# Optimization experiments

Hardware: AMD Instinct MI355X
Metric: run time of the kernel (lower is better)

The kernel has to match this reference:

```python
import jax, jax.numpy as jnp
import numpy as np

H = 64
IN_DIM = 32
N = 50000
E = 100000
B = 500


def setup_inputs() -> dict:
    key = jax.random.key(0)
    ks = jax.random.split(key, 16)
    def rn(k, shape, s=0.05):
        return jax.random.normal(k, shape, dtype=jnp.float32) * s
    inp = dict(
        nfeat=rn(ks[0], (N, IN_DIM), 1.0),
        efeat=rn(ks[1], (E, 5), 1.0),
        lin0_w=rn(ks[2], (IN_DIM, H)), lin0_b=jnp.zeros((H,), jnp.float32),
        ew1=rn(ks[3], (5, 128)), eb1=jnp.zeros((128,), jnp.float32),
        ew2=rn(ks[4], (128, H * H)), eb2=jnp.zeros((H * H,), jnp.float32),
        conv_b=jnp.zeros((H,), jnp.float32),
        gru_wih=rn(ks[5], (3 * H, H)), gru_whh=rn(ks[6], (3 * H, H)),
        gru_bih=jnp.zeros((3 * H,), jnp.float32), gru_bhh=jnp.zeros((3 * H,), jnp.float32),
        lstm_wih=rn(ks[7], (4 * H, 2 * H)), lstm_whh=rn(ks[8], (4 * H, H)),
        lstm_bih=jnp.zeros((4 * H,), jnp.float32), lstm_bhh=jnp.zeros((4 * H,), jnp.float32),
        fc1_w=rn(ks[9], (2 * H, H)), fc1_b=jnp.zeros((H,), jnp.float32),
        fc2_w=rn(ks[10], (H, 1)), fc2_b=jnp.zeros((1,), jnp.float32),
        src=jax.random.randint(ks[11], (E,), 0, N),
        dst=jax.random.randint(ks[12], (E,), 0, N),
        graph_id=jnp.arange(N) // (N // B),  # B graphs of equal size, sorted
        num_graphs=B,
    )
    return inp


def reference(nfeat, efeat, lin0_w, lin0_b, ew1, eb1, ew2, eb2, conv_b,
              gru_wih, gru_whh, gru_bih, gru_bhh,
              lstm_wih, lstm_whh, lstm_bih, lstm_bhh,
              fc1_w, fc1_b, fc2_w, fc2_b,
              src, dst, graph_id, num_graphs):
    n_nodes = nfeat.shape[0]
    # lin0 + relu
    h = jax.nn.relu(nfeat @ lin0_w + lin0_b)  # [N, H]
    # edge-conditioned weight matrices (same for all 3 iterations)
    We = (jax.nn.relu(efeat @ ew1 + eb1) @ ew2 + eb2).reshape(-1, H, H)  # [E, H, H]
    deg = jnp.maximum(
        jax.ops.segment_sum(jnp.ones(src.shape[0], jnp.float32), dst, num_segments=n_nodes), 1.0)
    for _ in range(3):
        # NNConv: gather src feats, per-edge matmul, scatter-mean at dst
        msg = jnp.einsum('eh,eho->eo', h[src], We)  # [E, H]
        agg = jax.ops.segment_sum(msg, dst, num_segments=n_nodes) / deg[:, None]
        m = jax.nn.relu(agg + conv_b)
        # GRU step (PyTorch gate order r,z,n)
        gi = m @ gru_wih.T + gru_bih
        gh = h @ gru_whh.T + gru_bhh
        r = jax.nn.sigmoid(gi[:, :H] + gh[:, :H])
        z = jax.nn.sigmoid(gi[:, H:2 * H] + gh[:, H:2 * H])
        n = jnp.tanh(gi[:, 2 * H:] + r * gh[:, 2 * H:])
        h = (1.0 - z) * n + z * h
    feat = h  # [N, H]
    # Set2Set pooling: 3 iters, 1-layer LSTM with input 2H
    q_star = jnp.zeros((num_graphs, 2 * H), jnp.float32)
    hh = jnp.zeros((num_graphs, H), jnp.float32)
    cc = jnp.zeros((num_graphs, H), jnp.float32)
    for _ in range(3):
        gates = q_star @ lstm_wih.T + lstm_bih + hh @ lstm_whh.T + lstm_bhh
        i = jax.nn.sigmoid(gates[:, :H])
        f = jax.nn.sigmoid(gates[:, H:2 * H])
        g = jnp.tanh(gates[:, 2 * H:3 * H])
        o = jax.nn.sigmoid(gates[:, 3 * H:])
        cc = f * cc + i * g
        hh = o * jnp.tanh(cc)
        q = hh  # [B, H]
        e = jnp.sum(feat * q[graph_id], axis=-1)  # [N]
        emax = jax.ops.segment_max(e, graph_id, num_segments=num_graphs)
        alpha = jnp.exp(e - emax[graph_id])
        denom = jax.ops.segment_sum(alpha, graph_id, num_segments=num_graphs)
        alpha = alpha / denom[graph_id]
        readout = jax.ops.segment_sum(alpha[:, None] * feat, graph_id, num_segments=num_graphs)
        q_star = jnp.concatenate([q, readout], axis=-1)  # [B, 2H]
    pred = jax.nn.relu(q_star @ fc1_w + fc1_b) @ fc2_w + fc2_b  # [B, 1]
    return pred.reshape(-1)
```

## Files before the change

kernel.cpp:

```cpp
#include <hip/hip_runtime.h>

#define HD 64
#define NNODE 50000
#define NEDGE 100000
#define NGR 500
#define NPG 100
#define EPAD 100352
#define NCH 66
#define NUPL 65

typedef _Float16 f16;
typedef _Float16 f16x2 __attribute__((ext_vector_type(2)));
typedef _Float16 f16x8 __attribute__((ext_vector_type(8)));
typedef float f32x4 __attribute__((ext_vector_type(4)));

__device__ __forceinline__ float sigmoidf_(float x) { return 1.f / (1.f + __expf(-x)); }

__device__ __forceinline__ void gload16(const void* g, void* l) {
    __builtin_amdgcn_global_load_lds((const __attribute__((address_space(1))) unsigned int*)g,
                                     (__attribute__((address_space(3))) unsigned int*)l, 16, 0, 0);
}

#define G_NODE 12500
#define G_EMLP 392
#define G_PACK 66
#define G_GRU  48
#define G_T1   128
#define G_T2   64
#define G_IDX  392
#define G_ALL (G_NODE + G_EMLP + G_PACK + G_GRU + G_T1 + G_T2 + G_IDX)

__global__ __launch_bounds__(256) void k_prep_all(
    const float* __restrict__ nfeat, const float* __restrict__ lin0_w, const float* __restrict__ lin0_b,
    const float* __restrict__ efeat, const float* __restrict__ ew1, const float* __restrict__ eb1,
    const float* __restrict__ ew2, const float* __restrict__ eb2,
    const float* __restrict__ gwih, const float* __restrict__ gwhh,
    const float* __restrict__ lwih, const float* __restrict__ lwhh,
    const int* __restrict__ src, const int* __restrict__ dst,
    float* __restrict__ h, f16x2* __restrict__ uP, f16* __restrict__ w2hp,
    f16* __restrict__ gB1, f16* __restrict__ gB2,
    float* __restrict__ lwihT, float* __restrict__ lwhhT,
    int* __restrict__ srcP, int* __restrict__ dstP, int* __restrict__ cnt) {
    __shared__ float sw[5 * 128];
    __shared__ float sb[128];
    __shared__ float s[8192];
    int bb = blockIdx.x;
    int t = threadIdx.x;
    if (bb < G_NODE) {
        int idx = bb * 256 + t;
        int n = idx >> 6, o = idx & 63;
        if (n >= NNODE) return;
        const float* nf = nfeat + n * 32;
        float acc = lin0_b[o];
#pragma unroll
        for (int i = 0; i < 32; i++) acc += nf[i] * lin0_w[i * 64 + o];
        h[idx] = fmaxf(acc, 0.f);
        return;
    }
    bb -= G_NODE;
    if (bb < G_EMLP) {
        for (int idx = t; idx < 640; idx += 256) sw[idx] = ew1[idx];
        if (t < 128) sb[t] = eb1[t];
        __syncthreads();
        int e = bb * 256 + t;
        bool valid = e < NEDGE;
        float ef[5];
#pragma unroll
        for (int i = 0; i < 5; i++) ef[i] = valid ? efeat[e * 5 + i] : 0.f;
#pragma unroll 2
        for (int c = 0; c < 64; c++) {
            float v[2];
#pragma unroll
            for (int ss = 0; ss < 2; ss++) {
                int k = 2 * c + ss;
                float acc = sb[k];
#pragma unroll
                for (int i = 0; i < 5; i++) acc += ef[i] * sw[i * 128 + k];
                v[ss] = valid ? fmaxf(acc, 0.f) : 0.f;
            }
            f16x2 pv;
            pv[0] = (f16)v[0];
            pv[1] = (f16)v[1];
            uP[(size_t)c * EPAD + e] = pv;
        }
        {
            f16x2 pv;
            pv[0] = valid ? (f16)1.f : (f16)0.f;
            pv[1] = pv[0];
            uP[(size_t)64 * EPAD + e] = pv;
        }
        return;
    }
    bb -= G_EMLP;
    if (bb < G_PACK) {
        int c = bb;
        for (int i = t; i < 8192; i += 256) {
            int kg = c * 128 + (i >> 6);
            float v = 0.f;
            if (kg < 8192) v = ew2[(size_t)c * 8192 + i];
            else if (kg < 8256) v = eb2[(kg - 8192) * 64 + (i & 63)];
            s[i] = v;
        }
        __syncthreads();
        f16* outp = w2hp + (size_t)c * 8192 + t * 32;
#pragma unroll
        for (int ff = 0; ff < 4; ff++) {
            int F = t * 4 + ff;
            int l = F & 63;
            int jj = (F >> 6) & 3;
            int sl = (F >> 8) & 3;
            f16x8 v;
#pragma unroll
            for (int q = 0; q < 8; q++)
                v[q] = (f16)s[(sl * 32 + ((l >> 4) << 3) + q) * 64 + jj * 16 + (l & 15)];
            *(f16x8*)(outp + ff * 8) = v;
        }
        return;
    }
    bb -= G_PACK;
    if (bb < G_GRU) {
        int idx = bb * 256 + t;
        int cp = idx >> 6, k = idx & 63;
        int w = cp / 48, rem = cp % 48;
        int tg = rem >> 4, cc = rem & 15;
        int orow = tg * 64 + w * 16 + cc;
        gB1[idx] = (f16)gwih[orow * 64 + k];
        gB2[idx] = (f16)gwhh[orow * 64 + k];
        return;
    }
    bb -= G_GRU;
    if (bb < G_T1) {
        int idx = bb * 256 + t;
        int r = idx >> 7, c = idx & 127;
        lwihT[c * 256 + r] = lwih[idx];
        return;
    }
    bb -= G_T1;
    if (bb < G_T2) {
        int idx = bb * 256 + t;
        int r = idx >> 6, c = idx & 63;
        lwhhT[c * 256 + r] = lwhh[idx];
        return;
    }
    bb -= G_T2;
    {
        int e = bb * 256 + t;
        if (e >= EPAD) return;
        if (e < NEDGE) {
            int d = dst[e];
            srcP[e] = src[e];
            dstP[e] = d;
            atomicAdd(&cnt[d], 1);
        } else {
            srcP[e] = 0;
            dstP[e] = -1;
        }
    }
}

__global__ __launch_bounds__(256) void k_msg(
    const float* __restrict__ h, const f16x2* __restrict__ uP, const f16* __restrict__ w2hp,
    const int* __restrict__ srcP, const int* __restrict__ dstP, float* __restrict__ agg) {
    __shared__ __attribute__((aligned(16))) f16 sB[2 * 16384];
    int t = threadIdx.x;
    int w = t >> 6, l = t & 63;
    int eb = blockIdx.x * 256 + w * 64;
    int lr = l & 15, lg = l >> 4;
    f16x8 xf[4][2];
#pragma unroll
    for (int i = 0; i < 4; i++) {
        const float* xb = h + (size_t)srcP[eb + i * 16 + lr] * 64;
#pragma unroll
        for (int p = 0; p < 2; p++) {
            float4 v0 = *(const float4*)(xb + p * 32 + lg * 8);
            float4 v1 = *(const float4*)(xb + p * 32 + lg * 8 + 4);
            f16x8 xv;
            xv[0] = (f16)v0.x; xv[1] = (f16)v0.y; xv[2] = (f16)v0.z; xv[3] = (f16)v0.w;
            xv[4] = (f16)v1.x; xv[5] = (f16)v1.y; xv[6] = (f16)v1.z; xv[7] = (f16)v1.w;
            xf[i][p] = xv;
        }
    }
    const f16x8* gB = (const f16x8*)w2hp;
    f16x8* sB8 = (f16x8*)sB;
#pragma unroll
    for (int i = 0; i < 8; i++)
        gload16(gB + i * 256 + t, sB8 + i * 256 + t);
    f32x4 acc[4][4];
#pragma unroll
    for (int i = 0; i < 4; i++)
#pragma unroll
        for (int j = 0; j < 4; j++) acc[i][j] = (f32x4){0.f, 0.f, 0.f, 0.f};
    f16x2 uc0[4], uc1[4], un0[4], un1[4];
#pragma unroll
    for (int i = 0; i < 4; i++) {
        uc0[i] = uP[eb + i * 16 + lr];
        uc1[i] = uP[(size_t)EPAD + eb + i * 16 + lr];
    }
    __syncthreads();
#pragma unroll 1
    for (int p = 0; p <= 32; p++) {
        int buf = p & 1;
        if (p < 32) {
            const f16x8* gs = gB + (size_t)(p + 1) * 2048;
            f16x8* ld = sB8 + (buf ^ 1) * 2048;
#pragma unroll
            for (int i = 0; i < 8; i++)
                gload16(gs + i * 256 + t, ld + i * 256 + t);
            int c0 = min(2 * p + 2, 64), c1 = min(2 * p + 3, 64);
#pragma unroll
            for (int i = 0; i < 4; i++) {
                un0[i] = uP[(size_t)c0 * EPAD + eb + i * 16 + lr];
                un1[i] = uP[(size_t)c1 * EPAD + eb + i * 16 + lr];
            }
        }
        {
            f16x8 bf[4][4];
#pragma unroll
            for (int s = 0; s < 4; s++)
#pragma unroll
                for (int j = 0; j < 4; j++)
                    bf[s][j] = sB8[buf * 2048 + s * 256 + j * 64 + l];
            __builtin_amdgcn_s_setprio(1);
#pragma unroll
            for (int s = 0; s < 4; s++)
#pragma unroll
                for (int i = 0; i < 4; i++) {
                    f16x8 av = xf[i][s & 1] * uc0[i][s >> 1];
#pragma unroll
                    for (int j = 0; j < 4; j++)
                        acc[i][j] = __builtin_amdgcn_mfma_f32_16x16x32_f16(av, bf[s][j], acc[i][j], 0, 0, 0);
                }
            __builtin_amdgcn_s_setprio(0);
        }
        {
            f16x8 bf[4][4];
#pragma unroll
            for (int s = 0; s < 4; s++)
#pragma unroll
                for (int j = 0; j < 4; j++)
                    bf[s][j] = sB8[buf * 2048 + 1024 + s * 256 + j * 64 + l];
            __builtin_amdgcn_s_setprio(1);
#pragma unroll
            for (int s = 0; s < 4; s++)
#pragma unroll
                for (int i = 0; i < 4; i++) {
                    f16x8 av = xf[i][s & 1] * uc1[i][s >> 1];
#pragma unroll
                    for (int j = 0; j < 4; j++)
                        acc[i][j] = __builtin_amdgcn_mfma_f32_16x16x32_f16(av, bf[s][j], acc[i][j], 0, 0, 0);
                }
            __builtin_amdgcn_s_setprio(0);
        }
#pragma unroll
        for (int i = 0; i < 4; i++) { uc0[i] = un0[i]; uc1[i] = un1[i]; }
        __syncthreads();
    }
#pragma unroll
    for (int i = 0; i < 4; i++) {
        int rb = eb + i * 16 + lg * 4;
        int4 d4 = *(const int4*)(dstP + rb);
#pragma unroll
        for (int r = 0; r < 4; r++) {
            int d = (r == 0) ? d4.x : (r == 1) ? d4.y : (r == 2) ? d4.z : d4.w;
            if (d >= 0) {
                float* ap = agg + (size_t)d * 64 + lr;
#pragma unroll
                for (int j = 0; j < 4; j++) atomicAdd(ap + j * 16, acc[i][j][r]);
            }
        }
    }
}

#define GWP 72
__global__ __launch_bounds__(256) void k_gru2(float* __restrict__ agg,
                                              const int* __restrict__ cnt,
                                              const float* __restrict__ convb,
                                              const f16* __restrict__ B1g,
                                              const f16* __restrict__ B2g,
                                              const float* __restrict__ bih,
                                              const float* __restrict__ bhh,
                                              float* __restrict__ h, int zero_agg) {
    __shared__ f16 sM[64 * GWP];
    __shared__ f16 sH[64 * GWP];
    int t = threadIdx.x;
    int nb = blockIdx.x * 64;
    int w = t >> 6, l = t & 63, lr = l & 15, lg = l >> 4;
    f16x8 b1[2][3], b2[2][3];
#pragma unroll
    for (int kk = 0; kk < 2; kk++)
#pragma unroll
        for (int j = 0; j < 3; j++) {
            size_t off = (size_t)(w * 48 + j * 16 + lr) * 64 + kk * 32 + lg * 8;
            b1[kk][j] = *(const f16x8*)(B1g + off);
            b2[kk][j] = *(const f16x8*)(B2g + off);
        }
#pragma unroll
    for (int it = 0; it < 16; it++) {
        int idx = t + 256 * it;
        int node = idx >> 6, k = idx & 63;
        int gn = nb + node;
        float mv = 0.f, hv = 0.f;
        if (gn < NNODE) {
            size_t off = (size_t)gn * 64 + k;
            float dinv = 1.f / (float)max(cnt[gn], 1);
            mv = fmaxf(agg[off] * dinv + convb[k], 0.f);
            hv = h[off];
            if (zero_agg) agg[off] = 0.f;
        }
        sM[node * GWP + k] = (f16)mv;
        sH[node * GWP + k] = (f16)hv;
    }
    __syncthreads();
    f32x4 aih[4][3], ahh[4][3];
#pragma unroll
    for (int i = 0; i < 4; i++)
#pragma unroll
        for (int j = 0; j < 3; j++) {
            aih[i][j] = (f32x4){0.f, 0.f, 0.f, 0.f};
            ahh[i][j] = (f32x4){0.f, 0.f, 0.f, 0.f};
        }
#pragma unroll
    for (int kk = 0; kk < 2; kk++) {
        f16x8 am[4], ah[4];
#pragma unroll
        for (int i = 0; i < 4; i++) {
            am[i] = *(const f16x8*)(sM + (i * 16 + lr) * GWP + kk * 32 + lg * 8);
            ah[i] = *(const f16x8*)(sH + (i * 16 + lr) * GWP + kk * 32 + lg * 8);
        }
#pragma unroll
        for (int i = 0; i < 4; i++)
#pragma unroll
            for (int j = 0; j < 3; j++) {
                aih[i][j] = __builtin_amdgcn_mfma_f32_16x16x32_f16(am[i], b1[kk][j], aih[i][j], 0, 0, 0);
                ahh[i][j] = __builtin_amdgcn_mfma_f32_16x16x32_f16(ah[i], b2[kk][j], ahh[i][j], 0, 0, 0);
            }
    }
    float bi0 = bih[0 * 64 + w * 16 + lr], bh0 = bhh[0 * 64 + w * 16 + lr];
    float bi1 = bih[1 * 64 + w * 16 + lr], bh1 = bhh[1 * 64 + w * 16 + lr];
    float bi2 = bih[2 * 64 + w * 16 + lr], bh2 = bhh[2 * 64 + w * 16 + lr];
#pragma unroll
    for (int i = 0; i < 4; i++)
#pragma unroll
        for (int r = 0; r < 4; r++) {
            int node = i * 16 + lg * 4 + r;
            int gn = nb + node;
            if (gn >= NNODE) continue;
            float rg = sigmoidf_(aih[i][0][r] + bi0 + ahh[i][0][r] + bh0);
            float z = sigmoidf_(aih[i][1][r] + bi1 + ahh[i][1][r] + bh1);
            float nn = tanhf(aih[i][2][r] + bi2 + rg * (ahh[i][2][r] + bh2));
            size_t off = (size_t)gn * 64 + w * 16 + lr;
            float hold = h[off];
            h[off] = (1.f - z) * nn + z * hold;
        }
}

#define FP 68
__global__ __launch_bounds__(256) void k_s2s(const float* __restrict__ feat,
                                             const float* __restrict__ wihT,
                                             const float* __restrict__ whhT,
                                             const float* __restrict__ lbih,
                                             const float* __restrict__ lbhh,
                                             const float* __restrict__ fc1w,
                                             const float* __restrict__ fc1b,
                                             const float* __restrict__ fc2w,
                                             const float* __restrict__ fc2b,
                                             float* __restrict__ out) {
    __shared__ float sf[NPG * FP];
    __shared__ float sq[128];
    __shared__ float sh[64], scc[64];
    __shared__ float sg[256];
    __shared__ float se[NPG];
    __shared__ float red[2];
    int g = blockIdx.x, t = threadIdx.x;
    const float* fb = feat + (size_t)g * NPG * 64;
    for (int idx = t; idx < NPG * 64; idx += 256)
        sf[(idx >> 6) * FP + (idx & 63)] = fb[idx];
    if (t < 128) sq[t] = 0.f;
    if (t >= 128 && t < 192) { sh[t - 128] = 0.f; scc[t - 128] = 0.f; }
    __syncthreads();
    for (int it = 0; it < 3; it++) {
        float gate = lbih[t] + lbhh[t];
#pragma unroll 8
        for (int i = 0; i < 128; i++) gate += sq[i] * wihT[i * 256 + t];
#pragma unroll 8
        for (int i = 0; i < 64; i++) gate += sh[i] * whhT[i * 256 + t];
        sg[t] = gate;
        __syncthreads();
        if (t < 64) {
            float ig = sigmoidf_(sg[t]);
            float fg = sigmoidf_(sg[64 + t]);
            float gg = tanhf(sg[128 + t]);
            float og = sigmoidf_(sg[192 + t]);
            float c = fg * scc[t] + ig * gg;
            scc[t] = c;
            float hv = og * tanhf(c);
            sh[t] = hv;
            sq[t] = hv;
        }
        __syncthreads();
        if (t < NPG) {
            float e = 0.f;
#pragma unroll 8
            for (int o = 0; o < 64; o++) e += sf[t * FP + o] * sh[o];
            se[t] = e;
        }
        __syncthreads();
        if (t < 64) {
            float m = -1e30f;
            for (int i2 = t; i2 < NPG; i2 += 64) m = fmaxf(m, se[i2]);
            for (int d = 32; d; d >>= 1) m = fmaxf(m, __shfl_down(m, d));
            if (t == 0) red[0] = m;
        }
        __syncthreads();
        float emax = red[0];
        if (t < NPG) se[t] = __expf(se[t] - emax);
        __syncthreads();
        if (t < 64) {
            float s = 0.f;
            for (int i2 = t; i2 < NPG; i2 += 64) s += se[i2];
            for (int d = 32; d; d >>= 1) s += __shfl_down(s, d);
            if (t == 0) red[1] = s;
        }
        __syncthreads();
        if (t < 64) {
            float dnv = 1.f / red[1];
            float r = 0.f;
#pragma unroll 4
            for (int n = 0; n < NPG; n++) r += se[n] * sf[n * FP + t];
            sq[64 + t] = r * dnv;
        }
        __syncthreads();
    }
    if (t < 64) {
        float hsum = fc1b[t];
#pragma unroll 8
        for (int i = 0; i < 128; i++) hsum += sq[i] * fc1w[i * 64 + t];
        float p = fmaxf(hsum, 0.f) * fc2w[t];
        for (int d = 32; d; d >>= 1) p += __shfl_down(p, d);
        if (t == 0) out[g] = p + fc2b[0];
    }
}

extern "C" void kernel_launch(void* const* d_in, const int* in_sizes, int n_in,
                              void* d_out, int out_size, void* d_ws, size_t ws_size,
                              hipStream_t stream) {
    const float* nfeat = (const float*)d_in[0];
    const float* efeat = (const float*)d_in[1];
    const float* lin0_w = (const float*)d_in[2];
    const float* lin0_b = (const float*)d_in[3];
    const float* ew1 = (const float*)d_in[4];
    const float* eb1 = (const float*)d_in[5];
    const float* ew2 = (const float*)d_in[6];
    const float* eb2 = (const float*)d_in[7];
    const float* convb = (const float*)d_in[8];
    const float* gwih = (const float*)d_in[9];
    const float* gwhh = (const float*)d_in[10];
    const float* gbih = (const float*)d_in[11];
    const float* gbhh = (const float*)d_in[12];
    const float* lwih = (const float*)d_in[13];
    const float* lwhh = (const float*)d_in[14];
    const float* lbih = (const float*)d_in[15];
    const float* lbhh = (const float*)d_in[16];
    const float* fc1w = (const float*)d_in[17];
    const float* fc1b = (const float*)d_in[18];
    const float* fc2w = (const float*)d_in[19];
    const float* fc2b = (const float*)d_in[20];
    const int* src = (const int*)d_in[21];
    const int* dst = (const int*)d_in[22];
    float* out = (float*)d_out;

    char* p = (char*)d_ws;
    auto alloc = [&](size_t bytes) {
        char* q = p;
        p += (bytes + 255) & ~(size_t)255;
        return q;
    };
    f16x2* uP = (f16x2*)alloc((size_t)NUPL * EPAD * 4);
    f16* w2hp = (f16*)alloc((size_t)NCH * 8192 * 2);
    float* h = (float*)alloc((size_t)NNODE * 64 * 4);
    float* agg = (float*)alloc((size_t)NNODE * 64 * 4);
    int* cnt = (int*)alloc((size_t)NNODE * 4);
    float* lwihT = (float*)alloc((size_t)128 * 256 * 4);
    float* lwhhT = (float*)alloc((size_t)64 * 256 * 4);
    f16* gB1 = (f16*)alloc((size_t)12288 * 2);
    f16* gB2 = (f16*)alloc((size_t)12288 * 2);
    int* srcP = (int*)alloc((size_t)EPAD * 4);
    int* dstP = (int*)alloc((size_t)EPAD * 4);
    if ((size_t)(p - (char*)d_ws) > ws_size) return;

    hipMemsetAsync(cnt, 0, (size_t)NNODE * 4, stream);
    hipMemsetAsync(agg, 0, (size_t)NNODE * 64 * 4, stream);

    k_prep_all<<<G_ALL, 256, 0, stream>>>(nfeat, lin0_w, lin0_b, efeat, ew1, eb1, ew2, eb2,
                                          gwih, gwhh, lwih, lwhh, src, dst,
                                          h, uP, w2hp, gB1, gB2, lwihT, lwhhT, srcP, dstP, cnt);

    for (int it = 0; it < 3; it++) {
        k_msg<<<EPAD / 256, 256, 0, stream>>>(h, uP, w2hp, srcP, dstP, agg);
        k_gru2<<<(NNODE + 63) / 64, 256, 0, stream>>>(agg, cnt, convb, gB1, gB2, gbih, gbhh, h,
                                                      it < 2 ? 1 : 0);
    }
    k_s2s<<<NGR, 256, 0, stream>>>(h, lwihT, lwhhT, lbih, lbhh, fc1w, fc1b, fc2w, fc2b, out);
}
```

Before: 470.5 us.

## Split k_msg output columns across two blocks to double grid and halve LDS

Each block of the message kernel now computes only half of the 64 output columns (32), chosen by the low bit of blockIdx. The grid doubles, shared-memory staging of the weight tiles halves, and the accumulator registers halve. This is meant to raise occupancy and spread the work over more CUs. In exchange, every edge's gathered source features and u coefficients are loaded twice and the A-operand scaling is recomputed in both halves.

```diff
diff --git a/kernel.cpp b/kernel.cpp
--- a/kernel.cpp
+++ b/kernel.cpp
@@ -161,10 +161,12 @@
 __global__ __launch_bounds__(256) void k_msg(
     const float* __restrict__ h, const f16x2* __restrict__ uP, const f16* __restrict__ w2hp,
     const int* __restrict__ srcP, const int* __restrict__ dstP, float* __restrict__ agg) {
-    __shared__ __attribute__((aligned(16))) f16 sB[2 * 16384];
+    __shared__ __attribute__((aligned(16))) f16 sB[2 * 8192];
     int t = threadIdx.x;
     int w = t >> 6, l = t & 63;
-    int eb = blockIdx.x * 256 + w * 64;
+    int bid = blockIdx.x;
+    int ch = bid & 1;
+    int eb = (bid >> 1) * 256 + w * 64;
     int lr = l & 15, lg = l >> 4;
     f16x8 xf[4][2];
 #pragma unroll
@@ -182,14 +184,25 @@
     }
     const f16x8* gB = (const f16x8*)w2hp;
     f16x8* sB8 = (f16x8*)sB;
-#pragma unroll
-    for (int i = 0; i < 8; i++)
-        gload16(gB + i * 256 + t, sB8 + i * 256 + t);
-    f32x4 acc[4][4];
-#pragma unroll
-    for (int i = 0; i < 4; i++)
-#pragma unroll
-        for (int j = 0; j < 4; j++) acc[i][j] = (f32x4){0.f, 0.f, 0.f, 0.f};
+#define STAGE_PAIR(PAIR, LDSBASE)                                                       \
+    {                                                                                   \
+        _Pragma("unroll") for (int q = 0; q < 2; q++) {                                 \
+            size_t cbase = ((size_t)(PAIR) * 2 + q) * 1024;                             \
+            _Pragma("unroll") for (int i2 = 0; i2 < 2; i2++) {                          \
+                int s2 = t + 256 * i2;                                                  \
+                int sl = s2 >> 7, jj2 = (s2 >> 6) & 1;                                  \
+                gload16(gB + cbase + sl * 256 + (2 * ch + jj2) * 64 + (s2 & 63),        \
+                        sB8 + (LDSBASE) + q * 512 + s2);                                \
+            }                                                                           \
+        }                                                                               \
+    }
+    STAGE_PAIR(0, 0)
+    f32x4 acc[4][2];
+#pragma unroll
+    for (int i = 0; i < 4; i++) {
+        acc[i][0] = (f32x4){0.f, 0.f, 0.f, 0.f};
+        acc[i][1] = (f32x4){0.f, 0.f, 0.f, 0.f};
+    }
     f16x2 uc0[4], uc1[4], un0[4], un1[4];
 #pragma unroll
     for (int i = 0; i < 4; i++) {
@@ -201,11 +214,7 @@
     for (int p = 0; p <= 32; p++) {
         int buf = p & 1;
         if (p < 32) {
-            const f16x8* gs = gB + (size_t)(p + 1) * 2048;
-            f16x8* ld = sB8 + (buf ^ 1) * 2048;
-#pragma unroll
-            for (int i = 0; i < 8; i++)
-                gload16(gs + i * 256 + t, ld + i * 256 + t);
+            STAGE_PAIR(p + 1, (buf ^ 1) * 1024)
             int c0 = min(2 * p + 2, 64), c1 = min(2 * p + 3, 64);
 #pragma unroll
             for (int i = 0; i < 4; i++) {
@@ -213,41 +222,23 @@
                 un1[i] = uP[(size_t)c1 * EPAD + eb + i * 16 + lr];
             }
         }
-        {
-            f16x8 bf[4][4];
+#pragma unroll
+        for (int q = 0; q < 2; q++) {
+            f16x8 bf[4][2];
 #pragma unroll
             for (int s = 0; s < 4; s++)
 #pragma unroll
-                for (int j = 0; j < 4; j++)
-                    bf[s][j] = sB8[buf * 2048 + s * 256 + j * 64 + l];
+                for (int j = 0; j < 2; j++)
+                    bf[s][j] = sB8[buf * 1024 + q * 512 + s * 128 + j * 64 + l];
             __builtin_amdgcn_s_setprio(1);
 #pragma unroll
             for (int s = 0; s < 4; s++)
 #pragma unroll
                 for (int i = 0; i < 4; i++) {
-                    f16x8 av = xf[i][s & 1] * uc0[i][s >> 1];
-#pragma unroll
-                    for (int j = 0; j < 4; j++)
-                        acc[i][j] = __builtin_amdgcn_mfma_f32_16x16x32_f16(av, bf[s][j], acc[i][j], 0, 0, 0);
-                }
-            __builtin_amdgcn_s_setprio(0);
-        }
-        {
-            f16x8 bf[4][4];
-#pragma unroll
-            for (int s = 0; s < 4; s++)
-#pragma unroll
-                for (int j = 0; j < 4; j++)
-                    bf[s][j] = sB8[buf * 2048 + 1024 + s * 256 + j * 64 + l];
-            __builtin_amdgcn_s_setprio(1);
-#pragma unroll
-            for (int s = 0; s < 4; s++)
-#pragma unroll
-                for (int i = 0; i < 4; i++) {
-                    f16x8 av = xf[i][s & 1] * uc1[i][s >> 1];
-#pragma unroll
-                    for (int j = 0; j < 4; j++)
-                        acc[i][j] = __builtin_amdgcn_mfma_f32_16x16x32_f16(av, bf[s][j], acc[i][j], 0, 0, 0);
+                    f16 uu = (q == 0) ? uc0[i][s >> 1] : uc1[i][s >> 1];
+                    f16x8 av = xf[i][s & 1] * uu;
+                    acc[i][0] = __builtin_amdgcn_mfma_f32_16x16x32_f16(av, bf[s][0], acc[i][0], 0, 0, 0);
+                    acc[i][1] = __builtin_amdgcn_mfma_f32_16x16x32_f16(av, bf[s][1], acc[i][1], 0, 0, 0);
                 }
             __builtin_amdgcn_s_setprio(0);
         }
@@ -263,9 +254,9 @@
         for (int r = 0; r < 4; r++) {
             int d = (r == 0) ? d4.x : (r == 1) ? d4.y : (r == 2) ? d4.z : d4.w;
             if (d >= 0) {
-                float* ap = agg + (size_t)d * 64 + lr;
-#pragma unroll
-                for (int j = 0; j < 4; j++) atomicAdd(ap + j * 16, acc[i][j][r]);
+                float* ap = agg + (size_t)d * 64 + ch * 32 + lr;
+                atomicAdd(ap, acc[i][0][r]);
+                atomicAdd(ap + 16, acc[i][1][r]);
             }
         }
     }
@@ -496,7 +487,7 @@
                                           h, uP, w2hp, gB1, gB2, lwihT, lwhhT, srcP, dstP, cnt);
 
     for (int it = 0; it < 3; it++) {
-        k_msg<<<EPAD / 256, 256, 0, stream>>>(h, uP, w2hp, srcP, dstP, agg);
+        k_msg<<<(EPAD / 256) * 2, 256, 0, stream>>>(h, uP, w2hp, srcP, dstP, agg);
         k_gru2<<<(NNODE + 63) / 64, 256, 0, stream>>>(agg, cnt, convb, gB1, gB2, gbih, gbhh, h,
                                                       it < 2 ? 1 : 0);
     }
```

Measured after the change: 520.1 us. 10.5% more time.

## Switch edge message kernel to 32x32x16 MFMA tiles with repacked weights

Applied to the files above, without the earlier changes.

Replaces the 16x16x32 f16 MFMA tiling in the per-edge message kernel with 32x32x16 MFMA, using 2x2 tiles of 32 edges by 32 outputs per wave. The weight packing in the prep kernel is changed to match the new B-fragment layout, and the source-feature gather and atomic scatter are reindexed for the 32x32 accumulator layout. The aim is fewer MFMA instructions and fewer LDS fragment reads per unit of work, at the cost of larger accumulator registers and a different atomic access pattern.

```diff
diff --git a/kernel.cpp b/kernel.cpp
--- a/kernel.cpp
+++ b/kernel.cpp
@@ -13,6 +13,7 @@
 typedef _Float16 f16x2 __attribute__((ext_vector_type(2)));
 typedef _Float16 f16x8 __attribute__((ext_vector_type(8)));
 typedef float f32x4 __attribute__((ext_vector_type(4)));
+typedef float f32x16 __attribute__((ext_vector_type(16)));
 
 __device__ __forceinline__ float sigmoidf_(float x) { return 1.f / (1.f + __expf(-x)); }
 
@@ -107,12 +108,12 @@
         for (int ff = 0; ff < 4; ff++) {
             int F = t * 4 + ff;
             int l = F & 63;
-            int jj = (F >> 6) & 3;
-            int sl = (F >> 8) & 3;
+            int jj = (F >> 6) & 1;
+            int sl = F >> 7;
             f16x8 v;
 #pragma unroll
             for (int q = 0; q < 8; q++)
-                v[q] = (f16)s[(sl * 32 + ((l >> 4) << 3) + q) * 64 + jj * 16 + (l & 15)];
+                v[q] = (f16)s[(sl * 16 + ((l >> 5) << 3) + q) * 64 + jj * 32 + (l & 31)];
             *(f16x8*)(outp + ff * 8) = v;
         }
         return;
@@ -165,19 +166,19 @@
     int t = threadIdx.x;
     int w = t >> 6, l = t & 63;
     int eb = blockIdx.x * 256 + w * 64;
-    int lr = l & 15, lg = l >> 4;
-    f16x8 xf[4][2];
-#pragma unroll
-    for (int i = 0; i < 4; i++) {
-        const float* xb = h + (size_t)srcP[eb + i * 16 + lr] * 64;
-#pragma unroll
-        for (int p = 0; p < 2; p++) {
-            float4 v0 = *(const float4*)(xb + p * 32 + lg * 8);
-            float4 v1 = *(const float4*)(xb + p * 32 + lg * 8 + 4);
+    int lm = l & 31, hi = l >> 5;
+    f16x8 xf[2][4];
+#pragma unroll
+    for (int i = 0; i < 2; i++) {
+        const float* xb = h + (size_t)srcP[eb + i * 32 + lm] * 64;
+#pragma unroll
+        for (int h4 = 0; h4 < 4; h4++) {
+            float4 v0 = *(const float4*)(xb + h4 * 16 + hi * 8);
+            float4 v1 = *(const float4*)(xb + h4 * 16 + hi * 8 + 4);
             f16x8 xv;
             xv[0] = (f16)v0.x; xv[1] = (f16)v0.y; xv[2] = (f16)v0.z; xv[3] = (f16)v0.w;
             xv[4] = (f16)v1.x; xv[5] = (f16)v1.y; xv[6] = (f16)v1.z; xv[7] = (f16)v1.w;
-            xf[i][p] = xv;
+            xf[i][h4] = xv;
         }
     }
     const f16x8* gB = (const f16x8*)w2hp;
@@ -185,16 +186,14 @@
 #pragma unroll
     for (int i = 0; i < 8; i++)
         gload16(gB + i * 256 + t, sB8 + i * 256 + t);
-    f32x4 acc[4][4];
-#pragma unroll
-    for (int i = 0; i < 4; i++)
-#pragma unroll
-        for (int j = 0; j < 4; j++) acc[i][j] = (f32x4){0.f, 0.f, 0.f, 0.f};
-    f16x2 uc0[4], uc1[4], un0[4], un1[4];
-#pragma unroll
-    for (int i = 0; i < 4; i++) {
-        uc0[i] = uP[eb + i * 16 + lr];
-        uc1[i] = uP[(size_t)EPAD + eb + i * 16 + lr];
+    f32x16 acc00, acc01, acc10, acc11;
+#pragma unroll
+    for (int r = 0; r < 16; r++) { acc00[r] = 0.f; acc01[r] = 0.f; acc10[r] = 0.f; acc11[r] = 0.f; }
+    f16x2 uc0[2], uc1[2], un0[2], un1[2];
+#pragma unroll
+    for (int i = 0; i < 2; i++) {
+        uc0[i] = uP[eb + i * 32 + lm];
+        uc1[i] = uP[(size_t)EPAD + eb + i * 32 + lm];
     }
     __syncthreads();
 #pragma unroll 1
@@ -208,64 +207,48 @@
                 gload16(gs + i * 256 + t, ld + i * 256 + t);
             int c0 = min(2 * p + 2, 64), c1 = min(2 * p + 3, 64);
 #pragma unroll
-            for (int i = 0; i < 4; i++) {
-                un0[i] = uP[(size_t)c0 * EPAD + eb + i * 16 + lr];
-                un1[i] = uP[(size_t)c1 * EPAD + eb + i * 16 + lr];
+            for (int i = 0; i < 2; i++) {
+                un0[i] = uP[(size_t)c0 * EPAD + eb + i * 32 + lm];
+                un1[i] = uP[(size_t)c1 * EPAD + eb + i * 32 + lm];
             }
         }
-        {
-            f16x8 bf[4][4];
-#pragma unroll
-            for (int s = 0; s < 4; s++)
-#pragma unroll
-                for (int j = 0; j < 4; j++)
-                    bf[s][j] = sB8[buf * 2048 + s * 256 + j * 64 + l];
+#pragma unroll
+        for (int q = 0; q < 2; q++) {
             __builtin_amdgcn_s_setprio(1);
 #pragma unroll
-            for (int s = 0; s < 4; s++)
-#pragma unroll
-                for (int i = 0; i < 4; i++) {
-                    f16x8 av = xf[i][s & 1] * uc0[i][s >> 1];
-#pragma unroll
-                    for (int j = 0; j < 4; j++)
-                        acc[i][j] = __builtin_amdgcn_mfma_f32_16x16x32_f16(av, bf[s][j], acc[i][j], 0, 0, 0);
+            for (int s = 0; s < 8; s++) {
+                f16x8 bf0 = sB8[buf * 2048 + q * 1024 + s * 128 + l];
+                f16x8 bf1 = sB8[buf * 2048 + q * 1024 + s * 128 + 64 + l];
+                f16 u0 = (q == 0) ? uc0[0][s >> 2] : uc1[0][s >> 2];
+                f16 u1 = (q == 0) ? uc0[1][s >> 2] : uc1[1][s >> 2];
+                f16x8 av0 = xf[0][s & 3] * u0;
+                f16x8 av1 = xf[1][s & 3] * u1;
+                acc00 = __builtin_amdgcn_mfma_f32_32x32x16_f16(av0, bf0, acc00, 0, 0, 0);
+                acc01 = __builtin_amdgcn_mfma_f32_32x32x16_f16(av0, bf1, acc01, 0, 0, 0);
+                acc10 = __builtin_amdgcn_mfma_f32_32x32x16_f16(av1, bf0, acc10, 0, 0, 0);
+                acc11 = __builtin_amdgcn_mfma_f32_32x32x16_f16(av1, bf1, acc11, 0, 0, 0);
+            }
+            __builtin_amdgcn_s_setprio(0);
+        }
+#pragma unroll
+        for (int i = 0; i < 2; i++) { uc0[i] = un0[i]; uc1[i] = un1[i]; }
+        __syncthreads();
+    }
+#pragma unroll
+    for (int i = 0; i < 2; i++) {
+#pragma unroll
+        for (int b = 0; b < 4; b++) {
+            int4 d4 = *(const int4*)(dstP + eb + i * 32 + 8 * b + 4 * hi);
+#pragma unroll
+            for (int rr = 0; rr < 4; rr++) {
+                int d = (rr == 0) ? d4.x : (rr == 1) ? d4.y : (rr == 2) ? d4.z : d4.w;
+                if (d >= 0) {
+                    float v0 = (i == 0) ? acc00[b * 4 + rr] : acc10[b * 4 + rr];
+                    float v1 = (i == 0) ? acc01[b * 4 + rr] : acc11[b * 4 + rr];
+                    float* ap = agg + (size_t)d * 64 + lm;
+                    atomicAdd(ap, v0);
+                    atomicAdd(ap + 32, v1);
                 }
-            __builtin_amdgcn_s_setprio(0);
-        }
-        {
-            f16x8 bf[4][4];
-#pragma unroll
-            for (int s = 0; s < 4; s++)
-#pragma unroll
-                for (int j = 0; j < 4; j++)
-                    bf[s][j] = sB8[buf * 2048 + 1024 + s * 256 + j * 64 + l];
-            __builtin_amdgcn_s_setprio(1);
-#pragma unroll
-            for (int s = 0; s < 4; s++)
-#pragma unroll
-                for (int i = 0; i < 4; i++) {
-                    f16x8 av = xf[i][s & 1] * uc1[i][s >> 1];
-#pragma unroll
-                    for (int j = 0; j < 4; j++)
-                        acc[i][j] = __builtin_amdgcn_mfma_f32_16x16x32_f16(av, bf[s][j], acc[i][j], 0, 0, 0);
-                }
-            __builtin_amdgcn_s_setprio(0);
-        }
-#pragma unroll
-        for (int i = 0; i < 4; i++) { uc0[i] = un0[i]; uc1[i] = un1[i]; }
-        __syncthreads();
-    }
-#pragma unroll
-    for (int i = 0; i < 4; i++) {
-        int rb = eb + i * 16 + lg * 4;
-        int4 d4 = *(const int4*)(dstP + rb);
-#pragma unroll
-        for (int r = 0; r < 4; r++) {
-            int d = (r == 0) ? d4.x : (r == 1) ? d4.y : (r == 2) ? d4.z : d4.w;
-            if (d >= 0) {
-                float* ap = agg + (size_t)d * 64 + lr;
-#pragma unroll
-                for (int j = 0; j < 4; j++) atomicAdd(ap + j * 16, acc[i][j][r]);
             }
         }
     }
```

New measurement: 504.7 us. +7.2%, slower.
